# Kernel tuning notes

Measured on AMD Instinct MI355X. Metric: run time of the kernel, lower is better.

The kernel has to match this reference:

```python
import jax, jax.numpy as jnp
import numpy as np
import math

B, T, J, D = 16, 243, 24, 256
H, W = 8, 4  # num_heads, half-window


def setup_inputs() -> dict:
    key = jax.random.key(0)
    k1, k2 = jax.random.split(key, 2)
    x_tan_seq = jax.random.normal(k1, (B, T, J, D), dtype=jnp.float32)
    W_qkv = jax.random.normal(k2, (3 * D, D), dtype=jnp.float32) * 0.02
    b_qkv = jnp.zeros((3 * D,), dtype=jnp.float32)
    tau = jnp.ones((H,), dtype=jnp.float32)
    return {"x_tan_seq": x_tan_seq, "W_qkv": W_qkv, "b_qkv": b_qkv, "tau": tau}


def reference(x_tan_seq, W_qkv, b_qkv, tau):
    Bb, Tt, Jj, Dd = x_tan_seq.shape
    d_h = Dd // H
    KW = 2 * W + 1
    # [B,T,J,D] -> [B*J, T, D]
    x = x_tan_seq.transpose(0, 2, 1, 3).reshape(Bb * Jj, Tt, Dd)
    # fused qkv projection (torch Linear: x @ W.T + b)
    qkv = x @ W_qkv.T + b_qkv                      # [BJ, T, 3D]
    qkv = qkv.reshape(Bb * Jj, Tt, 3, H, d_h)
    q = qkv[:, :, 0].transpose(0, 2, 1, 3)          # [BJ, H, T, dh]
    k = qkv[:, :, 1].transpose(0, 2, 1, 3)
    v = qkv[:, :, 2].transpose(0, 2, 1, 3)
    # replicate-pad time axis, then gather sliding windows
    k_pad = jnp.pad(k, ((0, 0), (0, 0), (W, W), (0, 0)), mode='edge')
    v_pad = jnp.pad(v, ((0, 0), (0, 0), (W, W), (0, 0)), mode='edge')
    idx = jnp.arange(Tt)[:, None] + jnp.arange(KW)[None, :]  # [T, KW] into padded axis
    k_win = k_pad[:, :, idx, :]                    # [BJ, H, T, KW, dh]
    v_win = v_pad[:, :, idx, :]
    tau_c = jnp.clip(tau, 0.001)[None, :, None, None]  # clamp(min=0.001)
    logits = jnp.einsum('bhtd,bhtkd->bhtk', q, k_win) / (math.sqrt(d_h) * tau_c)
    # mask out-of-bounds (replicated) frames
    frame = jnp.arange(Tt)[:, None] + (jnp.arange(KW)[None, :] - W)
    oob = (frame < 0) | (frame >= Tt)              # [T, KW]
    logits = jnp.where(oob[None, None], -jnp.inf, logits)
    attn = jax.nn.softmax(logits, axis=-1)
    agg = jnp.einsum('bhtk,bhtkd->bhtd', attn, v_win)  # [BJ, H, T, dh]
    out = agg.transpose(0, 2, 1, 3).reshape(Bb, Jj, Tt, Dd).transpose(0, 2, 1, 3)
    return out  # [B, T, J, D]
```

## Files before the change

### kernel.cpp

```cpp
#include <hip/hip_runtime.h>
#include <hip/hip_bf16.h>
#include <math.h>

typedef __hip_bfloat16 bf16;
typedef __attribute__((ext_vector_type(8))) short short8;
typedef __attribute__((ext_vector_type(4))) float float4v;

#define Tsz 243
#define Jsz 24
#define Dsz 256
#define Hsz 8
#define Wsz 4
#define KWsz 9
#define SEQ 384
#define Ksz 256
#define NBsz 96
#define JDsz 6144
#define LDA 40
#define MB 128
#define T0B 122

#define AS_BYTES (MB * LDA * 2)
#define BS_BYTES (NBsz * LDA * 2)
#define SMEM_BYTES 26112

#define LROW 17
#define KOFF (MB * LROW)
#define VOFF (2 * MB * LROW)

__device__ __forceinline__ bool tau_is_fp32(const void* tau) {
    return *(const unsigned int*)tau == 0x3F800000u;
}

__device__ __forceinline__ unsigned int pack2(float a, float b) {
    const unsigned int lo = (unsigned int)__builtin_bit_cast(unsigned short, __float2bfloat16(a));
    const unsigned int hi = (unsigned int)__builtin_bit_cast(unsigned short, __float2bfloat16(b));
    return lo | (hi << 16);
}
__device__ __forceinline__ float bflo(unsigned int p) { return __builtin_bit_cast(float, p << 16); }
__device__ __forceinline__ float bfhi(unsigned int p) { return __builtin_bit_cast(float, p & 0xffff0000u); }

__global__ __launch_bounds__(512, 6)
void fused_qkv_attn(const void* __restrict__ xp, const void* __restrict__ Wp,
                    const void* __restrict__ bp, const void* __restrict__ taup,
                    void* __restrict__ out)
{
    __shared__ __align__(16) char smem[SMEM_BYTES];
    bf16* As = (bf16*)smem;
    bf16* Bs = (bf16*)(smem + AS_BYTES);
    unsigned int*  ad  = (unsigned int*)smem;
    unsigned short* a16 = (unsigned short*)smem;

    const bool is32 = tau_is_fp32(taup);

    const int bid     = (int)blockIdx.x;
    const int logical = (bid & 7) * (SEQ * Hsz * 2 / 8) + (bid >> 3);
    const int s    = logical >> 4;
    const int h    = (logical >> 1) & 7;
    const int blk2 = logical & 1;
    const int b = s / Jsz;
    const int j = s - b * Jsz;
    const int r0 = blk2 ? (Tsz - MB) : 0;

    const int tid  = (int)threadIdx.x;
    const int wave = tid >> 6;
    const int lane = tid & 63;
    const int fr = lane & 15;
    const int fk = (lane >> 4) * 8;
    const int wm = wave * 16;

    const int arow  = tid >> 2;
    const int acol8 = (tid & 3) << 3;
    const size_t xrow = ((size_t)(b * Tsz + r0 + arow) * Jsz + j) * (size_t)Dsz;
    const float* xF = (const float*)xp + xrow + acol8;
    const bf16*  xB = (const bf16*) xp + xrow + acol8;
    bf16* aDst = As + arow * LDA + acol8;

    const int brow  = tid >> 2;
    const int bcol8 = (tid & 3) << 3;
    const int wrow  = ((brow >> 5) << 8) + (h << 5) + (brow & 31);
    const float* wF = (const float*)Wp + (size_t)wrow * Ksz + bcol8;
    const bf16*  wB = (const bf16*) Wp + (size_t)wrow * Ksz + bcol8;
    bf16* bDst = Bs + brow * LDA + bcol8;

    float4v acc[6];
#pragma unroll
    for (int n = 0; n < 6; ++n)
        acc[n] = (float4v){0.f, 0.f, 0.f, 0.f};

    for (int kt = 0; kt < Ksz; kt += 32) {
        if (is32) {
            const float4 a0 = *(const float4*)(xF + kt);
            const float4 a1 = *(const float4*)(xF + kt + 4);
            *(uint4*)aDst = make_uint4(pack2(a0.x,a0.y), pack2(a0.z,a0.w),
                                       pack2(a1.x,a1.y), pack2(a1.z,a1.w));
            if (tid < 384) {
                const float4 b0 = *(const float4*)(wF + kt);
                const float4 b1 = *(const float4*)(wF + kt + 4);
                *(uint4*)bDst = make_uint4(pack2(b0.x,b0.y), pack2(b0.z,b0.w),
                                           pack2(b1.x,b1.y), pack2(b1.z,b1.w));
            }
        } else {
            *(uint4*)aDst = *(const uint4*)(xB + kt);
            if (tid < 384)
                *(uint4*)bDst = *(const uint4*)(wB + kt);
        }
        __syncthreads();

        const short8 af = *(const short8*)(As + (wm + fr) * LDA + fk);
#pragma unroll
        for (int n = 0; n < 6; ++n) {
            const short8 bf = *(const short8*)(Bs + ((n << 4) + fr) * LDA + fk);
            acc[n] = __builtin_amdgcn_mfma_f32_16x16x32_bf16(af, bf, acc[n], 0, 0, 0);
        }
        __syncthreads();
    }

    const int r0acc = (lane >> 4) << 2;
#pragma unroll
    for (int n = 0; n < 6; ++n) {
        const int sec = n >> 1;
        const int d   = ((n & 1) << 4) + fr;
        const int bcol = (sec << 8) + (h << 5) + d;
        const float bv = is32 ? ((const float*)bp)[bcol]
                              : __bfloat162float(((const bf16*)bp)[bcol]);
        const int tbase = wm + r0acc;
#pragma unroll
        for (int r = 0; r < 4; ++r)
            a16[sec * (2 * KOFF) + (tbase + r) * (2 * LROW) + d] =
                __builtin_bit_cast(unsigned short, __float2bfloat16(acc[n][r] + bv));
    }
    __syncthreads();

    const int tq  = tid >> 2;
    const int qtr = tid & 3;
    const int nOut = blk2 ? (Tsz - T0B) : T0B;
    if (tq < nOut) {
        const int tOut = blk2 ? (T0B + tq) : tq;
        const int tlq  = tOut - r0;
        const int o4   = qtr << 2;

        const float tv = is32 ? ((const float*)taup)[h]
                              : __bfloat162float(((const bf16*)taup)[h]);
        const float scale = 1.0f / (5.656854249f * fmaxf(tv, 0.001f));

        float q[8];
#pragma unroll
        for (int u = 0; u < 4; ++u) {
            const unsigned int p = ad[tlq * LROW + o4 + u];
            q[2*u]   = bflo(p);
            q[2*u+1] = bfhi(p);
        }

        float wgt[KWsz];
        float mx = -1e30f;
#pragma unroll
        for (int w = 0; w < KWsz; ++w) {
            const int tp = tOut + w - Wsz;
            float sv = -1e30f;
            if (tp >= 0 && tp < Tsz) {
                const int tpl = tp - r0;
                float p0 = 0.f, p1 = 0.f;
#pragma unroll
                for (int u = 0; u < 4; ++u) {
                    const unsigned int pa = ad[KOFF + tpl * LROW + o4 + u];
                    p0 += q[2*u]   * bflo(pa);
                    p1 += q[2*u+1] * bfhi(pa);
                }
                float part = p0 + p1;
                part += __shfl_xor(part, 1, 64);
                part += __shfl_xor(part, 2, 64);
                sv = part * scale;
            }
            wgt[w] = sv;
            mx = fmaxf(mx, sv);
        }

        float den = 0.f;
#pragma unroll
        for (int w = 0; w < KWsz; ++w) {
            const float e = (wgt[w] > -1e29f) ? __expf(wgt[w] - mx) : 0.f;
            wgt[w] = e;
            den += e;
        }
        const float inv = 1.0f / fmaxf(den, 1e-30f);

        float o[8];
#pragma unroll
        for (int d = 0; d < 8; ++d) o[d] = 0.f;
#pragma unroll
        for (int w = 0; w < KWsz; ++w) {
            const int tp = tOut + w - Wsz;
            if (tp >= 0 && tp < Tsz) {
                const int tpl = tp - r0;
                const float a = wgt[w] * inv;
#pragma unroll
                for (int u = 0; u < 4; ++u) {
                    const unsigned int p = ad[VOFF + tpl * LROW + o4 + u];
                    o[2*u]   += a * bflo(p);
                    o[2*u+1] += a * bfhi(p);
                }
            }
        }

        const size_t ooff = ((size_t)(b * Tsz + tOut) * Jsz + j) * Dsz + (h << 5) + (qtr << 3);
        if (is32) {
            float* op = (float*)out + ooff;
            *(float4*)op       = make_float4(o[0], o[1], o[2], o[3]);
            *(float4*)(op + 4) = make_float4(o[4], o[5], o[6], o[7]);
        } else {
            unsigned int* op = (unsigned int*)((bf16*)out + ooff);
            *(uint4*)op = make_uint4(pack2(o[0],o[1]), pack2(o[2],o[3]),
                                     pack2(o[4],o[5]), pack2(o[6],o[7]));
        }
    }
}

extern "C" void kernel_launch(void* const* d_in, const int* in_sizes, int n_in,
                              void* d_out, int out_size, void* d_ws, size_t ws_size,
                              hipStream_t stream) {
    (void)in_sizes; (void)n_in; (void)out_size; (void)d_ws; (void)ws_size;
    fused_qkv_attn<<<SEQ * Hsz * 2, 512, 0, stream>>>(d_in[0], d_in[1], d_in[2], d_in[3], d_out);
}
```

Before: 270.2 us.

## Compute windowed attention with MFMA banded tiles instead of scalar per-thread loops

Replaces the scalar per-thread sliding-window dot products and weighted sum with MFMA tiles: each wave computes a 16x64 QK^T band, masks it to the 9-wide window, does softmax with cross-lane shuffles, writes bf16 probabilities to shared memory, and multiplies by a transposed V tile with MFMA. V is stored transposed in LDS, and the LDS footprint grows to about 47 KB. Most of the banded MFMA work falls on masked positions, and the larger LDS use may reduce occupancy. Output stores become scalar per element instead of vectorized float4, and probabilities are rounded to bf16.

```diff
diff --git a/kernel.cpp b/kernel.cpp
--- a/kernel.cpp
+++ b/kernel.cpp
@@ -21,12 +21,13 @@
 #define T0B 122
 
 #define AS_BYTES (MB * LDA * 2)
-#define BS_BYTES (NBsz * LDA * 2)
-#define SMEM_BYTES 26112
-
-#define LROW 17
-#define KOFF (MB * LROW)
-#define VOFF (2 * MB * LROW)
+
+#define KOFFs 5120
+#define VTOFFs 10240
+#define VTSTR 136
+#define POFFs 14592
+#define PSTR 72
+#define SMEM_BYTES 47616
 
 __device__ __forceinline__ bool tau_is_fp32(const void* tau) {
     return *(const unsigned int*)tau == 0x3F800000u;
@@ -37,8 +38,9 @@
     const unsigned int hi = (unsigned int)__builtin_bit_cast(unsigned short, __float2bfloat16(b));
     return lo | (hi << 16);
 }
-__device__ __forceinline__ float bflo(unsigned int p) { return __builtin_bit_cast(float, p << 16); }
-__device__ __forceinline__ float bfhi(unsigned int p) { return __builtin_bit_cast(float, p & 0xffff0000u); }
+__device__ __forceinline__ unsigned short bf16bits(float x) {
+    return __builtin_bit_cast(unsigned short, __float2bfloat16(x));
+}
 
 __global__ __launch_bounds__(512, 6)
 void fused_qkv_attn(const void* __restrict__ xp, const void* __restrict__ Wp,
@@ -48,8 +50,7 @@
     __shared__ __align__(16) char smem[SMEM_BYTES];
     bf16* As = (bf16*)smem;
     bf16* Bs = (bf16*)(smem + AS_BYTES);
-    unsigned int*  ad  = (unsigned int*)smem;
-    unsigned short* a16 = (unsigned short*)smem;
+    unsigned short* s16 = (unsigned short*)smem;
 
     const bool is32 = tau_is_fp32(taup);
 
@@ -118,7 +119,7 @@
 
     const int r0acc = (lane >> 4) << 2;
 #pragma unroll
-    for (int n = 0; n < 6; ++n) {
+    for (int n = 0; n < 4; ++n) {
         const int sec = n >> 1;
         const int d   = ((n & 1) << 4) + fr;
         const int bcol = (sec << 8) + (h << 5) + d;
@@ -127,91 +128,99 @@
         const int tbase = wm + r0acc;
 #pragma unroll
         for (int r = 0; r < 4; ++r)
-            a16[sec * (2 * KOFF) + (tbase + r) * (2 * LROW) + d] =
-                __builtin_bit_cast(unsigned short, __float2bfloat16(acc[n][r] + bv));
+            s16[sec * KOFFs + (tbase + r) * LDA + d] = bf16bits(acc[n][r] + bv);
+    }
+#pragma unroll
+    for (int n = 4; n < 6; ++n) {
+        const int d   = ((n & 1) << 4) + fr;
+        const int bcol = 512 + (h << 5) + d;
+        const float bv = is32 ? ((const float*)bp)[bcol]
+                              : __bfloat162float(((const bf16*)bp)[bcol]);
+#pragma unroll
+        for (int r = 0; r < 4; ++r)
+            s16[VTOFFs + d * VTSTR + (wm + r0acc + r)] = bf16bits(acc[n][r] + bv);
     }
     __syncthreads();
 
-    const int tq  = tid >> 2;
-    const int qtr = tid & 3;
-    const int nOut = blk2 ? (Tsz - T0B) : T0B;
-    if (tq < nOut) {
-        const int tOut = blk2 ? (T0B + tq) : tq;
-        const int tlq  = tOut - r0;
-        const int o4   = qtr << 2;
-
-        const float tv = is32 ? ((const float*)taup)[h]
-                              : __bfloat162float(((const bf16*)taup)[h]);
-        const float scale = 1.0f / (5.656854249f * fmaxf(tv, 0.001f));
-
-        float q[8];
-#pragma unroll
-        for (int u = 0; u < 4; ++u) {
-            const unsigned int p = ad[tlq * LROW + o4 + u];
-            q[2*u]   = bflo(p);
-            q[2*u+1] = bfhi(p);
-        }
-
-        float wgt[KWsz];
-        float mx = -1e30f;
-#pragma unroll
-        for (int w = 0; w < KWsz; ++w) {
-            const int tp = tOut + w - Wsz;
-            float sv = -1e30f;
-            if (tp >= 0 && tp < Tsz) {
-                const int tpl = tp - r0;
-                float p0 = 0.f, p1 = 0.f;
-#pragma unroll
-                for (int u = 0; u < 4; ++u) {
-                    const unsigned int pa = ad[KOFF + tpl * LROW + o4 + u];
-                    p0 += q[2*u]   * bflo(pa);
-                    p1 += q[2*u+1] * bfhi(pa);
-                }
-                float part = p0 + p1;
-                part += __shfl_xor(part, 1, 64);
-                part += __shfl_xor(part, 2, 64);
-                sv = part * scale;
+    const float tv = is32 ? ((const float*)taup)[h]
+                          : __bfloat162float(((const bf16*)taup)[h]);
+    const float scale = 1.0f / (5.656854249f * fmaxf(tv, 0.001f));
+    const int g  = wave;
+    const int wb = (g <= 1) ? 0 : ((g >= 5) ? 64 : ((g - 1) << 4));
+
+    const short8 qf = *(const short8*)((const bf16*)s16 + (g * 16 + fr) * LDA + fk);
+    float4v sacc[4];
+#pragma unroll
+    for (int s2 = 0; s2 < 4; ++s2) {
+        const short8 kf = *(const short8*)((const bf16*)s16 + KOFFs + (wb + s2 * 16 + fr) * LDA + fk);
+        sacc[s2] = __builtin_amdgcn_mfma_f32_16x16x32_bf16(qf, kf, (float4v){0.f,0.f,0.f,0.f}, 0, 0, 0);
+    }
+
+    float vv[4][4];
+    const int dly = (lane & 15) + wb - (g << 4) - r0acc;
+#pragma unroll
+    for (int s2 = 0; s2 < 4; ++s2)
+#pragma unroll
+        for (int r = 0; r < 4; ++r) {
+            const int dd = dly + s2 * 16 - r;
+            vv[s2][r] = ((unsigned)(dd + 4) <= 8u) ? sacc[s2][r] * scale : -1e30f;
+        }
+
+    float inv[4];
+#pragma unroll
+    for (int r = 0; r < 4; ++r) {
+        float m = fmaxf(fmaxf(vv[0][r], vv[1][r]), fmaxf(vv[2][r], vv[3][r]));
+        m = fmaxf(m, __shfl_xor(m, 1, 64));
+        m = fmaxf(m, __shfl_xor(m, 2, 64));
+        m = fmaxf(m, __shfl_xor(m, 4, 64));
+        m = fmaxf(m, __shfl_xor(m, 8, 64));
+        float dsum = 0.f;
+#pragma unroll
+        for (int s2 = 0; s2 < 4; ++s2) {
+            vv[s2][r] = __expf(vv[s2][r] - m);
+            dsum += vv[s2][r];
+        }
+        dsum += __shfl_xor(dsum, 1, 64);
+        dsum += __shfl_xor(dsum, 2, 64);
+        dsum += __shfl_xor(dsum, 4, 64);
+        dsum += __shfl_xor(dsum, 8, 64);
+        inv[r] = 1.0f / fmaxf(dsum, 1e-30f);
+    }
+
+    unsigned short* pb = s16 + POFFs + g * (16 * PSTR);
+#pragma unroll
+    for (int s2 = 0; s2 < 4; ++s2)
+#pragma unroll
+        for (int r = 0; r < 4; ++r)
+            pb[(r0acc + r) * PSTR + s2 * 16 + (lane & 15)] = bf16bits(vv[s2][r] * inv[r]);
+
+    float4v oacc[2] = {(float4v){0.f,0.f,0.f,0.f}, (float4v){0.f,0.f,0.f,0.f}};
+#pragma unroll
+    for (int ks = 0; ks < 2; ++ks) {
+        const short8 pa = *(const short8*)((const bf16*)pb + fr * PSTR + ks * 32 + fk);
+#pragma unroll
+        for (int nt = 0; nt < 2; ++nt) {
+            const short8 vb = *(const short8*)((const bf16*)s16 + VTOFFs +
+                                               (nt * 16 + fr) * VTSTR + wb + ks * 32 + fk);
+            oacc[nt] = __builtin_amdgcn_mfma_f32_16x16x32_bf16(pa, vb, oacc[nt], 0, 0, 0);
+        }
+    }
+
+#pragma unroll
+    for (int r = 0; r < 4; ++r) {
+        const int tl   = (g << 4) + r0acc + r;
+        const int tOut = r0 + tl;
+        const bool own = blk2 ? (tOut >= T0B) : (tOut < T0B);
+        if (own) {
+            const size_t obase = ((size_t)(b * Tsz + tOut) * Jsz + j) * (size_t)Dsz
+                               + (h << 5) + (lane & 15);
+            if (is32) {
+                ((float*)out)[obase]      = oacc[0][r];
+                ((float*)out)[obase + 16] = oacc[1][r];
+            } else {
+                ((bf16*)out)[obase]      = __float2bfloat16(oacc[0][r]);
+                ((bf16*)out)[obase + 16] = __float2bfloat16(oacc[1][r]);
             }
-            wgt[w] = sv;
-            mx = fmaxf(mx, sv);
-        }
-
-        float den = 0.f;
-#pragma unroll
-        for (int w = 0; w < KWsz; ++w) {
-            const float e = (wgt[w] > -1e29f) ? __expf(wgt[w] - mx) : 0.f;
-            wgt[w] = e;
-            den += e;
-        }
-        const float inv = 1.0f / fmaxf(den, 1e-30f);
-
-        float o[8];
-#pragma unroll
-        for (int d = 0; d < 8; ++d) o[d] = 0.f;
-#pragma unroll
-        for (int w = 0; w < KWsz; ++w) {
-            const int tp = tOut + w - Wsz;
-            if (tp >= 0 && tp < Tsz) {
-                const int tpl = tp - r0;
-                const float a = wgt[w] * inv;
-#pragma unroll
-                for (int u = 0; u < 4; ++u) {
-                    const unsigned int p = ad[VOFF + tpl * LROW + o4 + u];
-                    o[2*u]   += a * bflo(p);
-                    o[2*u+1] += a * bfhi(p);
-                }
-            }
-        }
-
-        const size_t ooff = ((size_t)(b * Tsz + tOut) * Jsz + j) * Dsz + (h << 5) + (qtr << 3);
-        if (is32) {
-            float* op = (float*)out + ooff;
-            *(float4*)op       = make_float4(o[0], o[1], o[2], o[3]);
-            *(float4*)(op + 4) = make_float4(o[4], o[5], o[6], o[7]);
-        } else {
-            unsigned int* op = (unsigned int*)((bf16*)out + ooff);
-            *(uint4*)op = make_uint4(pack2(o[0],o[1]), pack2(o[2],o[3]),
-                                     pack2(o[4],o[5]), pack2(o[6],o[7]));
         }
     }
 }
```

Result: slower. 290.6 us (+7.6%).
